# Optimization experiments

Hardware: AMD Instinct MI355X
Metric: run time of the kernel (lower is better)

The kernel has to match this reference:

```python
import jax, jax.numpy as jnp
import numpy as np

NEG_SLOPE = 0.2  # PyG GATConv default leaky_relu slope


def add_self_loops(src, dst, ea, n_nodes):
    # PyG add_self_loops with fill_value='mean': self-loop attr = mean of
    # incoming edge attrs per destination node (0 if no incoming edges).
    cnt = jax.ops.segment_sum(jnp.ones(dst.shape, ea.dtype), dst, num_segments=n_nodes)
    mean_ea = jax.ops.segment_sum(ea, dst, num_segments=n_nodes) / jnp.maximum(cnt, 1.0)[:, None]
    loop = jnp.arange(n_nodes, dtype=src.dtype)
    return (jnp.concatenate([src, loop]),
            jnp.concatenate([dst, loop]),
            jnp.concatenate([ea, mean_ea], axis=0))


def gat_conv(x, src, dst, ea, W, att_src, att_dst, We, att_edge, bias, heads, ch, concat):
    n = x.shape[0]
    xs = (x @ W).reshape(n, heads, ch)                      # [N,H,C]
    a_src = (xs * att_src).sum(-1)                          # [N,H]
    a_dst = (xs * att_dst).sum(-1)                          # [N,H]
    ea_p = (ea @ We).reshape(-1, heads, ch)                 # [E,H,C]
    a_e = (ea_p * att_edge).sum(-1)                         # [E,H]
    logits = jax.nn.leaky_relu(a_src[src] + a_dst[dst] + a_e, NEG_SLOPE)
    m = jax.ops.segment_max(logits, dst, num_segments=n)    # segment softmax over dst
    e = jnp.exp(logits - m[dst])
    denom = jax.ops.segment_sum(e, dst, num_segments=n)
    alpha = e / (denom[dst] + 1e-16)                        # [E,H]
    out = jax.ops.segment_sum(alpha[:, :, None] * xs[src], dst, num_segments=n)  # [N,H,C]
    out = out.reshape(n, heads * ch) if concat else out.mean(axis=1)
    return out + bias


def setup_inputs() -> dict:
    key = jax.random.key(0)
    ks = jax.random.split(key, 14)
    N, E, F_IN, H, C1, C2 = 50000, 800000, 128, 2, 64, 64
    s = 0.05
    return {
        "x": jax.random.normal(ks[0], (N, F_IN), jnp.float32),
        "edge_index": jax.random.randint(ks[1], (2, E), 0, N, jnp.int32),
        "edge_weight": jax.random.uniform(ks[2], (E,), jnp.float32),
        # layer 1 (heads=2, concat=True)
        "W1": jax.random.normal(ks[3], (F_IN, H * C1), jnp.float32) * s,
        "att_src1": jax.random.normal(ks[4], (1, H, C1), jnp.float32) * s,
        "att_dst1": jax.random.normal(ks[5], (1, H, C1), jnp.float32) * s,
        "We1": jax.random.normal(ks[6], (1, H * C1), jnp.float32) * s,
        "att_edge1": jax.random.normal(ks[7], (1, H, C1), jnp.float32) * s,
        "b1": jnp.zeros((H * C1,), jnp.float32),
        # layer 2 (heads=1, concat=False)
        "W2": jax.random.normal(ks[8], (H * C1, C2), jnp.float32) * s,
        "att_src2": jax.random.normal(ks[9], (1, 1, C2), jnp.float32) * s,
        "att_dst2": jax.random.normal(ks[10], (1, 1, C2), jnp.float32) * s,
        "We2": jax.random.normal(ks[11], (1, C2), jnp.float32) * s,
        "att_edge2": jax.random.normal(ks[12], (1, 1, C2), jnp.float32) * s,
        "b2": jnp.zeros((C2,), jnp.float32),
    }


def reference(x, edge_index, edge_weight, W1, att_src1, att_dst1, We1, att_edge1, b1,
              W2, att_src2, att_dst2, We2, att_edge2, b2):
    n = x.shape[0]
    ea = edge_weight[:, None]  # edge_dim=1
    src, dst, ea = add_self_loops(edge_index[0], edge_index[1], ea, n)
    h = gat_conv(x, src, dst, ea, W1, att_src1, att_dst1, We1, att_edge1, b1,
                 heads=2, ch=64, concat=True)
    h = jax.nn.elu(h)
    out = gat_conv(h, src, dst, ea, W2, att_src2, att_dst2, We2, att_edge2, b2,
                   heads=1, ch=64, concat=False)
    return out
```

## Files before the change

kernel.cpp:

```cpp
#include <hip/hip_runtime.h>
#include <math.h>

#define NEG_SLOPE 0.2f

typedef unsigned int u32;
typedef unsigned short u16;
typedef unsigned long long u64;

typedef __attribute__((ext_vector_type(8))) short short8;
typedef __attribute__((ext_vector_type(4))) float f32x4;

__device__ __forceinline__ float bf2f(u16 h) {
  union { u32 u; float f; } c; c.u = ((u32)h) << 16; return c.f;
}
__device__ __forceinline__ u16 f2bf(float f) {
  union { float f; u32 u; } c; c.f = f;
  return (u16)((c.u + 0x7FFFu + ((c.u >> 16) & 1u)) >> 16);
}

__global__ __launch_bounds__(256) void k_hist(const int* __restrict__ dst, int E, int epb,
                                              u32* __restrict__ hist) {
  __shared__ u32 h[256];
  h[threadIdx.x] = 0;
  __syncthreads();
  int b = blockIdx.x;
  int beg = b * epb, end = beg + epb; if (end > E) end = E;
  for (int i = beg + threadIdx.x; i < end; i += 256)
    atomicAdd(&h[(u32)dst[i] >> 8], 1u);
  __syncthreads();
  hist[threadIdx.x * 256 + b] = h[threadIdx.x];
}

__global__ __launch_bounds__(256) void k_scanrow(u32* __restrict__ hist, u32* __restrict__ btot) {
  int bkt = blockIdx.x, t = threadIdx.x;
  u32 orig = hist[bkt * 256 + t];
  u32 v = orig;
  #pragma unroll
  for (int off = 1; off < 64; off <<= 1) {
    u32 u_ = __shfl_up(v, off);
    if ((t & 63) >= off) v += u_;
  }
  __shared__ u32 ws[4];
  if ((t & 63) == 63) ws[t >> 6] = v;
  __syncthreads();
  u32 add = 0; int w = t >> 6;
  if (w > 0) add += ws[0];
  if (w > 1) add += ws[1];
  if (w > 2) add += ws[2];
  u32 incl = v + add;
  hist[bkt * 256 + t] = incl - orig;
  if (t == 255) btot[bkt] = incl;
}

__global__ __launch_bounds__(256) void k_scanb(const u32* __restrict__ btot, u32* __restrict__ bstart) {
  int t = threadIdx.x;
  u32 orig = btot[t];
  u32 v = orig;
  #pragma unroll
  for (int off = 1; off < 64; off <<= 1) {
    u32 u_ = __shfl_up(v, off);
    if ((t & 63) >= off) v += u_;
  }
  __shared__ u32 ws[4];
  if ((t & 63) == 63) ws[t >> 6] = v;
  __syncthreads();
  u32 add = 0; int w = t >> 6;
  if (w > 0) add += ws[0];
  if (w > 1) add += ws[1];
  if (w > 2) add += ws[2];
  u32 incl = v + add;
  bstart[t] = incl - orig;
  if (t == 255) bstart[256] = incl;
}

__global__ __launch_bounds__(256) void k_binscatter(const int* __restrict__ src,
                                                    const int* __restrict__ dst,
                                                    const float* __restrict__ ew,
                                                    const u32* __restrict__ hist,
                                                    const u32* __restrict__ bstart,
                                                    u64* __restrict__ stage, int E, int epb) {
  __shared__ u32 cur[256];
  int b = blockIdx.x;
  cur[threadIdx.x] = bstart[threadIdx.x] + hist[threadIdx.x * 256 + b];
  __syncthreads();
  int beg = b * epb, end = beg + epb; if (end > E) end = E;
  for (int i = beg + threadIdx.x; i < end; i += 256) {
    int d = dst[i];
    u32 bkt = (u32)d >> 8;
    u32 pos = atomicAdd(&cur[bkt], 1u);
    float w = ew[i];
    u32 wq = (u32)(w * 65536.0f); if (wq > 65535u) wq = 65535u;
    stage[pos] = ((u64)((u32)d & 255u) << 32) | ((u64)wq << 16) | (u64)(u32)src[i];
  }
}

__global__ __launch_bounds__(256) void k_bucket(const u64* __restrict__ stage,
                                                const u32* __restrict__ bstart,
                                                u32* __restrict__ col,
                                                u32* __restrict__ ninfo, int n) {
  int bkt = blockIdx.x;
  int beg = (int)bstart[bkt], end = (int)bstart[bkt + 1];
  __shared__ u32 cnt[256];
  __shared__ u32 wsum[256];
  __shared__ u32 cur[256];
  cnt[threadIdx.x] = 0; wsum[threadIdx.x] = 0; cur[threadIdx.x] = 0;
  __syncthreads();
  for (int i = beg + threadIdx.x; i < end; i += 256) {
    u64 sv = stage[i];
    u32 ln = (u32)(sv >> 32) & 255u;
    atomicAdd(&cnt[ln], 1u);
    atomicAdd(&wsum[ln], (u32)((sv >> 16) & 0xFFFFu));
  }
  __syncthreads();
  int v = (bkt << 8) + threadIdx.x;
  if (v < n) {
    u32 deg = cnt[threadIdx.x];
    float mean = ((float)wsum[threadIdx.x] * (1.0f / 65536.0f)) / (float)(deg > 1 ? deg : 1);
    u32 mq = (u32)(mean * 65536.0f); if (mq > 65535u) mq = 65535u;
    u32 dc = deg > 64u ? 64u : deg;
    ninfo[v] = (dc << 16) | mq;
  }
  __syncthreads();
  for (int i = beg + threadIdx.x; i < end; i += 256) {
    u64 sv = stage[i];
    u32 ln = (u32)(sv >> 32) & 255u;
    u32 rank = atomicAdd(&cur[ln], 1u);
    if (rank < 64u)
      col[((((u32)bkt << 8) + ln) << 6) + rank] = (u32)sv;
  }
}

template<int H>
__global__ void k_bfrag(const float* __restrict__ W, uint4* __restrict__ bfrag) {
  int tid = blockIdx.x * 256 + threadIdx.x;
  int f = tid >> 6, lane = tid & 63;
  const int NF = H * 4 * 4 * 2;
  if (f >= NF) return;
  int p = f & 1, t = (f >> 1) & 3, cg = f >> 3;
  int colc = 16 * cg + (lane & 15);
  int k0 = 32 * t + 8 * (lane >> 4);
  u16 v[8];
  #pragma unroll
  for (int j = 0; j < 8; j++) {
    float w = W[(size_t)(k0 + j) * (H * 64) + colc];
    u32 bits = __float_as_uint(w);
    if (p == 0) v[j] = (u16)(bits >> 16);
    else        v[j] = f2bf(w - __uint_as_float(bits & 0xffff0000u));
  }
  uint4 o = { (u32)v[0] | ((u32)v[1] << 16), (u32)v[2] | ((u32)v[3] << 16),
              (u32)v[4] | ((u32)v[5] << 16), (u32)v[6] | ((u32)v[7] << 16) };
  bfrag[f * 64 + lane] = o;
}

template<int H>
__global__ __launch_bounds__(256) void k_gemm_mfma(const float* __restrict__ A,
                                                   const uint4* __restrict__ bfrag,
                                                   u16* __restrict__ xs_bf,
                                                   const float* __restrict__ att_src,
                                                   const float* __restrict__ att_dst,
                                                   float* __restrict__ a_src_out,
                                                   float* __restrict__ a_dst_out,
                                                   int nrows) {
  const int NCG = H * 4;
  int lane = threadIdx.x & 63;
  int wv = threadIdx.x >> 6;
  int lrow = lane & 15, lk = lane >> 4;
  int r0 = blockIdx.x * 64 + wv * 16;
  int arow = r0 + lrow; if (arow > nrows - 1) arow = nrows - 1;
  const float* ap = A + (size_t)arow * 128;

  f32x4 acc[NCG];
  #pragma unroll
  for (int cg = 0; cg < NCG; cg++) acc[cg] = (f32x4){0.f, 0.f, 0.f, 0.f};

  #pragma unroll
  for (int t = 0; t < 4; t++) {
    float4 av0 = *(const float4*)(ap + 32 * t + 8 * lk);
    float4 av1 = *(const float4*)(ap + 32 * t + 8 * lk + 4);
    float af[8] = {av0.x, av0.y, av0.z, av0.w, av1.x, av1.y, av1.z, av1.w};
    short8 ahi, alo;
    #pragma unroll
    for (int j = 0; j < 8; j++) {
      u32 bits = __float_as_uint(af[j]);
      ahi[j] = (short)(bits >> 16);
      alo[j] = (short)f2bf(af[j] - __uint_as_float(bits & 0xffff0000u));
    }
    #pragma unroll
    for (int cg = 0; cg < NCG; cg++) {
      union { uint4 u; short8 s; } bh, bl;
      bh.u = bfrag[((cg * 4 + t) * 2 + 0) * 64 + lane];
      bl.u = bfrag[((cg * 4 + t) * 2 + 1) * 64 + lane];
      acc[cg] = __builtin_amdgcn_mfma_f32_16x16x32_bf16(ahi, bh.s, acc[cg], 0, 0, 0);
      acc[cg] = __builtin_amdgcn_mfma_f32_16x16x32_bf16(ahi, bl.s, acc[cg], 0, 0, 0);
      acc[cg] = __builtin_amdgcn_mfma_f32_16x16x32_bf16(alo, bh.s, acc[cg], 0, 0, 0);
    }
  }

  float ps[2][4], pd[2][4];
  #pragma unroll
  for (int h = 0; h < 2; h++)
    #pragma unroll
    for (int r = 0; r < 4; r++) { ps[h][r] = 0.f; pd[h][r] = 0.f; }

  #pragma unroll
  for (int cg = 0; cg < NCG; cg++) {
    int colbase = 16 * cg + lrow;
    float asv = att_src[colbase];
    float adv = att_dst[colbase];
    const int h = (H == 2) ? (cg >> 2) : 0;
    #pragma unroll
    for (int r = 0; r < 4; r++) {
      ps[h][r] += acc[cg][r] * asv;
      pd[h][r] += acc[cg][r] * adv;
      int row = r0 + 4 * lk + r;
      if (row < nrows) xs_bf[(size_t)row * (H * 64) + colbase] = f2bf(acc[cg][r]);
    }
  }
  #pragma unroll
  for (int h = 0; h < H; h++)
    #pragma unroll
    for (int r = 0; r < 4; r++)
      #pragma unroll
      for (int off = 8; off; off >>= 1) {
        ps[h][r] += __shfl_xor(ps[h][r], off);
        pd[h][r] += __shfl_xor(pd[h][r], off);
      }
  if (lrow == 0) {
    #pragma unroll
    for (int r = 0; r < 4; r++) {
      int row = r0 + 4 * lk + r;
      if (row < nrows) {
        #pragma unroll
        for (int h = 0; h < H; h++) {
          a_src_out[row * H + h] = ps[h][r];
          a_dst_out[row * H + h] = pd[h][r];
        }
      }
    }
  }
}

__global__ void k_scalars(const float* __restrict__ We1, const float* __restrict__ ae1,
                          const float* __restrict__ We2, const float* __restrict__ ae2,
                          float* __restrict__ out) {
  int t = threadIdx.x;
  if (t == 0) { float s = 0; for (int c = 0; c < 64; c++) s += We1[c] * ae1[c]; out[0] = s; }
  if (t == 1) { float s = 0; for (int c = 0; c < 64; c++) s += We1[64 + c] * ae1[64 + c]; out[1] = s; }
  if (t == 2) { float s = 0; for (int c = 0; c < 64; c++) s += We2[c] * ae2[c]; out[2] = s; }
}

__global__ __launch_bounds__(256) void k_agg1(const u32* __restrict__ ninfo,
                                              const u32* __restrict__ col,
                                              const float2* __restrict__ a_src,
                                              const float2* __restrict__ a_dst,
                                              const float* __restrict__ scal,
                                              const u16* __restrict__ xs_bf,
                                              const float* __restrict__ b1,
                                              float* __restrict__ h_out, int n) {
  int wid = (blockIdx.x * 256 + threadIdx.x) >> 4;
  int gl = threadIdx.x & 15;
  if (wid >= n) return;
  u32 nf = ninfo[wid];
  int deg = (int)(nf >> 16);
  float mean = (float)(nf & 0xFFFFu) * (1.0f / 65536.0f);
  float2 ad = a_dst[wid];
  float2 asv_s = a_src[wid];
  float sc0 = scal[0], sc1 = scal[1];
  bool hi = gl >= 8;
  float l0s = asv_s.x + ad.x + mean * sc0;
  float l1s = asv_s.y + ad.y + mean * sc1;
  l0s = l0s > 0.f ? l0s : NEG_SLOPE * l0s;
  l1s = l1s > 0.f ? l1s : NEG_SLOPE * l1s;
  float m0 = l0s, m1 = l1s, den0 = 1.f, den1 = 1.f;
  float acc[8];
  {
    uint4 q = *(const uint4*)&xs_bf[(size_t)wid * 128 + 8 * gl];
    acc[0] = bf2f((u16)q.x); acc[1] = bf2f((u16)(q.x >> 16));
    acc[2] = bf2f((u16)q.y); acc[3] = bf2f((u16)(q.y >> 16));
    acc[4] = bf2f((u16)q.z); acc[5] = bf2f((u16)(q.z >> 16));
    acc[6] = bf2f((u16)q.w); acc[7] = bf2f((u16)(q.w >> 16));
  }
  const u32* cw = col + ((u32)wid << 6);
  for (int p0 = 0; p0 < deg; p0 += 16) {
    int p = p0 + gl;
    bool act = p < deg;
    u32 sw = cw[act ? p : 0];
    int s = (int)(sw & 0xFFFFu);
    float w = (float)(sw >> 16) * (1.0f / 65536.0f);
    float2 asv = a_src[s];
    float l0 = asv.x + ad.x + w * sc0;
    float l1 = asv.y + ad.y + w * sc1;
    l0 = l0 > 0.f ? l0 : NEG_SLOPE * l0;
    l1 = l1 > 0.f ? l1 : NEG_SLOPE * l1;
    if (!act) { l0 = -1e30f; l1 = -1e30f; }
    float cm0 = l0, cm1 = l1;
    #pragma unroll
    for (int off = 8; off; off >>= 1) {
      cm0 = fmaxf(cm0, __shfl_xor(cm0, off, 16));
      cm1 = fmaxf(cm1, __shfl_xor(cm1, off, 16));
    }
    float nm0 = fmaxf(m0, cm0), nm1 = fmaxf(m1, cm1);
    float e0 = __expf(l0 - nm0), e1 = __expf(l1 - nm1);
    float cs0 = e0, cs1 = e1;
    #pragma unroll
    for (int off = 8; off; off >>= 1) {
      cs0 += __shfl_xor(cs0, off, 16);
      cs1 += __shfl_xor(cs1, off, 16);
    }
    float r0 = __expf(m0 - nm0), r1 = __expf(m1 - nm1);
    den0 = den0 * r0 + cs0;
    den1 = den1 * r1 + cs1;
    float rs = hi ? r1 : r0;
    #pragma unroll
    for (int f = 0; f < 8; f++) acc[f] *= rs;
    m0 = nm0; m1 = nm1;
    int cnt = deg - p0; if (cnt > 16) cnt = 16;
    for (int j = 0; j < cnt; j++) {
      float a0 = __shfl(e0, j, 16);
      float a1 = __shfl(e1, j, 16);
      int   sj = __shfl(s, j, 16);
      uint4 q = *(const uint4*)&xs_bf[(size_t)sj * 128 + 8 * gl];
      float al = hi ? a1 : a0;
      acc[0] += al * bf2f((u16)q.x); acc[1] += al * bf2f((u16)(q.x >> 16));
      acc[2] += al * bf2f((u16)q.y); acc[3] += al * bf2f((u16)(q.y >> 16));
      acc[4] += al * bf2f((u16)q.z); acc[5] += al * bf2f((u16)(q.z >> 16));
      acc[6] += al * bf2f((u16)q.w); acc[7] += al * bf2f((u16)(q.w >> 16));
    }
  }
  float inv = 1.f / ((hi ? den1 : den0) + 1e-16f);
  float4 blo = *(const float4*)&b1[8 * gl];
  float4 bhi = *(const float4*)&b1[8 * gl + 4];
  float o[8];
  o[0] = acc[0] * inv + blo.x; o[1] = acc[1] * inv + blo.y;
  o[2] = acc[2] * inv + blo.z; o[3] = acc[3] * inv + blo.w;
  o[4] = acc[4] * inv + bhi.x; o[5] = acc[5] * inv + bhi.y;
  o[6] = acc[6] * inv + bhi.z; o[7] = acc[7] * inv + bhi.w;
  #pragma unroll
  for (int f = 0; f < 8; f++) o[f] = o[f] > 0.f ? o[f] : expm1f(o[f]);
  float* dst = &h_out[(size_t)wid * 128 + 8 * gl];
  *(float4*)dst = make_float4(o[0], o[1], o[2], o[3]);
  *(float4*)(dst + 4) = make_float4(o[4], o[5], o[6], o[7]);
}

__global__ __launch_bounds__(256) void k_agg2(const u32* __restrict__ ninfo,
                                              const u32* __restrict__ col,
                                              const float* __restrict__ a_src,
                                              const float* __restrict__ a_dst,
                                              const float* __restrict__ scal,
                                              const u16* __restrict__ xs_bf,
                                              const float* __restrict__ b2,
                                              float* __restrict__ out, int n) {
  int wid = (blockIdx.x * 256 + threadIdx.x) >> 3;
  int gl = threadIdx.x & 7;
  if (wid >= n) return;
  u32 nf = ninfo[wid];
  int deg = (int)(nf >> 16);
  float mean = (float)(nf & 0xFFFFu) * (1.0f / 65536.0f);
  float adv = a_dst[wid];
  float sc = scal[2];
  float ls = a_src[wid] + adv + mean * sc;
  ls = ls > 0.f ? ls : NEG_SLOPE * ls;
  float m = ls, den = 1.f;
  float acc[8];
  {
    uint4 q = *(const uint4*)&xs_bf[(size_t)wid * 64 + 8 * gl];
    acc[0] = bf2f((u16)q.x); acc[1] = bf2f((u16)(q.x >> 16));
    acc[2] = bf2f((u16)q.y); acc[3] = bf2f((u16)(q.y >> 16));
    acc[4] = bf2f((u16)q.z); acc[5] = bf2f((u16)(q.z >> 16));
    acc[6] = bf2f((u16)q.w); acc[7] = bf2f((u16)(q.w >> 16));
  }
  const u32* cw = col + ((u32)wid << 6);
  for (int p0 = 0; p0 < deg; p0 += 8) {
    int p = p0 + gl;
    bool act = p < deg;
    u32 sw = cw[act ? p : 0];
    int s = (int)(sw & 0xFFFFu);
    float w = (float)(sw >> 16) * (1.0f / 65536.0f);
    float l = a_src[s] + adv + w * sc;
    l = l > 0.f ? l : NEG_SLOPE * l;
    if (!act) l = -1e30f;
    float cm = l;
    #pragma unroll
    for (int off = 4; off; off >>= 1) cm = fmaxf(cm, __shfl_xor(cm, off, 8));
    float nm = fmaxf(m, cm);
    float e = __expf(l - nm);
    float cs = e;
    #pragma unroll
    for (int off = 4; off; off >>= 1) cs += __shfl_xor(cs, off, 8);
    float r = __expf(m - nm);
    den = den * r + cs;
    #pragma unroll
    for (int f = 0; f < 8; f++) acc[f] *= r;
    m = nm;
    int cnt = deg - p0; if (cnt > 8) cnt = 8;
    for (int j = 0; j < cnt; j++) {
      float aj = __shfl(e, j, 8);
      int   sj = __shfl(s, j, 8);
      uint4 q = *(const uint4*)&xs_bf[(size_t)sj * 64 + 8 * gl];
      acc[0] += aj * bf2f((u16)q.x); acc[1] += aj * bf2f((u16)(q.x >> 16));
      acc[2] += aj * bf2f((u16)q.y); acc[3] += aj * bf2f((u16)(q.y >> 16));
      acc[4] += aj * bf2f((u16)q.z); acc[5] += aj * bf2f((u16)(q.z >> 16));
      acc[6] += aj * bf2f((u16)q.w); acc[7] += aj * bf2f((u16)(q.w >> 16));
    }
  }
  float inv = 1.f / (den + 1e-16f);
  float4 blo = *(const float4*)&b2[8 * gl];
  float4 bhi = *(const float4*)&b2[8 * gl + 4];
  float* dst = &out[(size_t)wid * 64 + 8 * gl];
  *(float4*)dst = make_float4(acc[0] * inv + blo.x, acc[1] * inv + blo.y,
                              acc[2] * inv + blo.z, acc[3] * inv + blo.w);
  *(float4*)(dst + 4) = make_float4(acc[4] * inv + bhi.x, acc[5] * inv + bhi.y,
                                    acc[6] * inv + bhi.z, acc[7] * inv + bhi.w);
}

extern "C" void kernel_launch(void* const* d_in, const int* in_sizes, int n_in,
                              void* d_out, int out_size, void* d_ws, size_t ws_size,
                              hipStream_t stream) {
  const float* x   = (const float*)d_in[0];
  const int*   ei  = (const int*)d_in[1];
  const float* ew  = (const float*)d_in[2];
  const float* W1  = (const float*)d_in[3];
  const float* as1 = (const float*)d_in[4];
  const float* ad1 = (const float*)d_in[5];
  const float* We1 = (const float*)d_in[6];
  const float* ae1 = (const float*)d_in[7];
  const float* b1  = (const float*)d_in[8];
  const float* W2  = (const float*)d_in[9];
  const float* as2 = (const float*)d_in[10];
  const float* ad2 = (const float*)d_in[11];
  const float* We2 = (const float*)d_in[12];
  const float* ae2 = (const float*)d_in[13];
  const float* b2  = (const float*)d_in[14];

  const int n = in_sizes[0] / 128;
  const int E = in_sizes[1] / 2;
  const int epb = (E + 255) / 256;
  const int nbk = (n + 255) >> 8;

  char* wsb = (char*)d_ws;
  size_t off = 0;
  auto alloc = [&](size_t bytes) -> void* {
    void* p = wsb + off; off += (bytes + 255) & ~(size_t)255; return p;
  };
  u32*   hist    = (u32*)  alloc((size_t)256 * 256 * 4);
  u32*   btot    = (u32*)  alloc((size_t)256 * 4);
  u32*   bstart  = (u32*)  alloc((size_t)257 * 4);
  u64*   stage   = (u64*)  alloc((size_t)E * 8);
  u32*   col     = (u32*)  alloc((size_t)n * 64 * 4);
  u32*   ninfo   = (u32*)  alloc((size_t)n * 4);
  uint4* bfrag1  = (uint4*)alloc((size_t)64 * 64 * 16);
  uint4* bfrag2  = (uint4*)alloc((size_t)32 * 64 * 16);
  u16*   xs_bf   = (u16*)  alloc((size_t)n * 128 * 2);
  float* h1      = (float*)alloc((size_t)n * 128 * 4);
  float* a_src1v = (float*)alloc((size_t)n * 2 * 4);
  float* a_dst1v = (float*)alloc((size_t)n * 2 * 4);
  float* a_src2v = (float*)alloc((size_t)n * 4);
  float* a_dst2v = (float*)alloc((size_t)n * 4);
  float* scal    = (float*)alloc(64);
  if (off > ws_size) return;

  dim3 B(256);
  k_hist<<<dim3(256), B, 0, stream>>>(ei + E, E, epb, hist);
  k_scanrow<<<dim3(256), B, 0, stream>>>(hist, btot);
  k_scanb<<<dim3(1), B, 0, stream>>>(btot, bstart);
  k_binscatter<<<dim3(256), B, 0, stream>>>(ei, ei + E, ew, hist, bstart, stage, E, epb);
  k_bucket<<<dim3(nbk), B, 0, stream>>>(stage, bstart, col, ninfo, n);
  k_bfrag<2><<<dim3(16), B, 0, stream>>>(W1, bfrag1);
  k_bfrag<1><<<dim3(8), B, 0, stream>>>(W2, bfrag2);
  k_scalars<<<1, 64, 0, stream>>>(We1, ae1, We2, ae2, scal);
  k_gemm_mfma<2><<<dim3((n + 63) / 64), B, 0, stream>>>(x, bfrag1, xs_bf, as1, ad1,
                                                        a_src1v, a_dst1v, n);
  k_agg1<<<dim3((n + 15) / 16), B, 0, stream>>>(ninfo, col,
                                                (const float2*)a_src1v,
                                                (const float2*)a_dst1v,
                                                scal, xs_bf, b1, h1, n);
  k_gemm_mfma<1><<<dim3((n + 63) / 64), B, 0, stream>>>(h1, bfrag2, xs_bf, as2, ad2,
                                                        a_src2v, a_dst2v, n);
  k_agg2<<<dim3((n + 31) / 32), B, 0, stream>>>(ninfo, col, a_src2v, a_dst2v,
                                                scal, xs_bf, b2, (float*)d_out, n);
}
```

Measured before the change: 141.1 us.

## Fuse bucket count and scatter passes; unroll gather loops by two

The bucketing kernel now packs the degree count and the quantized weight sum into a single shared atomic per node. The returned old value gives the rank directly, which removes the second pass over the staged edges and one barrier. Both GAT aggregation kernels unroll the neighbor gather by two so that two independent row loads are in flight at once, raising memory-level parallelism. The packed counter limits the weight sum to 24 bits and the rank to 8 bits, so a node with about 256 or more incoming edges would overflow.

```diff
diff --git a/kernel.cpp b/kernel.cpp
--- a/kernel.cpp
+++ b/kernel.cpp
@@ -100,33 +100,27 @@
                                                 u32* __restrict__ ninfo, int n) {
   int bkt = blockIdx.x;
   int beg = (int)bstart[bkt], end = (int)bstart[bkt + 1];
-  __shared__ u32 cnt[256];
-  __shared__ u32 wsum[256];
-  __shared__ u32 cur[256];
-  cnt[threadIdx.x] = 0; wsum[threadIdx.x] = 0; cur[threadIdx.x] = 0;
+  __shared__ u32 pk[256];
+  pk[threadIdx.x] = 0;
   __syncthreads();
   for (int i = beg + threadIdx.x; i < end; i += 256) {
     u64 sv = stage[i];
     u32 ln = (u32)(sv >> 32) & 255u;
-    atomicAdd(&cnt[ln], 1u);
-    atomicAdd(&wsum[ln], (u32)((sv >> 16) & 0xFFFFu));
+    u32 wq = (u32)((sv >> 16) & 0xFFFFu);
+    u32 old = atomicAdd(&pk[ln], (1u << 24) | wq);
+    u32 rank = old >> 24;
+    if (rank < 64u)
+      col[((((u32)bkt << 8) + ln) << 6) + rank] = (u32)sv;
   }
   __syncthreads();
   int v = (bkt << 8) + threadIdx.x;
   if (v < n) {
-    u32 deg = cnt[threadIdx.x];
-    float mean = ((float)wsum[threadIdx.x] * (1.0f / 65536.0f)) / (float)(deg > 1 ? deg : 1);
+    u32 p = pk[threadIdx.x];
+    u32 deg = p >> 24;
+    float mean = ((float)(p & 0xFFFFFFu) * (1.0f / 65536.0f)) / (float)(deg > 1 ? deg : 1);
     u32 mq = (u32)(mean * 65536.0f); if (mq > 65535u) mq = 65535u;
     u32 dc = deg > 64u ? 64u : deg;
     ninfo[v] = (dc << 16) | mq;
-  }
-  __syncthreads();
-  for (int i = beg + threadIdx.x; i < end; i += 256) {
-    u64 sv = stage[i];
-    u32 ln = (u32)(sv >> 32) & 255u;
-    u32 rank = atomicAdd(&cur[ln], 1u);
-    if (rank < 64u)
-      col[((((u32)bkt << 8) + ln) << 6) + rank] = (u32)sv;
   }
 }
 
@@ -315,11 +309,29 @@
     for (int f = 0; f < 8; f++) acc[f] *= rs;
     m0 = nm0; m1 = nm1;
     int cnt = deg - p0; if (cnt > 16) cnt = 16;
-    for (int j = 0; j < cnt; j++) {
-      float a0 = __shfl(e0, j, 16);
-      float a1 = __shfl(e1, j, 16);
-      int   sj = __shfl(s, j, 16);
+    int j = 0;
+    for (; j + 2 <= cnt; j += 2) {
+      int sj0 = __shfl(s, j, 16);
+      int sj1 = __shfl(s, j + 1, 16);
+      uint4 qa = *(const uint4*)&xs_bf[(size_t)sj0 * 128 + 8 * gl];
+      uint4 qb = *(const uint4*)&xs_bf[(size_t)sj1 * 128 + 8 * gl];
+      float a0 = __shfl(e0, j, 16), a1 = __shfl(e1, j, 16);
+      float b0 = __shfl(e0, j + 1, 16), b1 = __shfl(e1, j + 1, 16);
+      float ala = hi ? a1 : a0;
+      float alb = hi ? b1 : b0;
+      acc[0] += ala * bf2f((u16)qa.x); acc[1] += ala * bf2f((u16)(qa.x >> 16));
+      acc[2] += ala * bf2f((u16)qa.y); acc[3] += ala * bf2f((u16)(qa.y >> 16));
+      acc[4] += ala * bf2f((u16)qa.z); acc[5] += ala * bf2f((u16)(qa.z >> 16));
+      acc[6] += ala * bf2f((u16)qa.w); acc[7] += ala * bf2f((u16)(qa.w >> 16));
+      acc[0] += alb * bf2f((u16)qb.x); acc[1] += alb * bf2f((u16)(qb.x >> 16));
+      acc[2] += alb * bf2f((u16)qb.y); acc[3] += alb * bf2f((u16)(qb.y >> 16));
+      acc[4] += alb * bf2f((u16)qb.z); acc[5] += alb * bf2f((u16)(qb.z >> 16));
+      acc[6] += alb * bf2f((u16)qb.w); acc[7] += alb * bf2f((u16)(qb.w >> 16));
+    }
+    if (j < cnt) {
+      int sj = __shfl(s, j, 16);
       uint4 q = *(const uint4*)&xs_bf[(size_t)sj * 128 + 8 * gl];
+      float a0 = __shfl(e0, j, 16), a1 = __shfl(e1, j, 16);
       float al = hi ? a1 : a0;
       acc[0] += al * bf2f((u16)q.x); acc[1] += al * bf2f((u16)(q.x >> 16));
       acc[2] += al * bf2f((u16)q.y); acc[3] += al * bf2f((u16)(q.y >> 16));
@@ -393,10 +405,27 @@
     for (int f = 0; f < 8; f++) acc[f] *= r;
     m = nm;
     int cnt = deg - p0; if (cnt > 8) cnt = 8;
-    for (int j = 0; j < cnt; j++) {
+    int j = 0;
+    for (; j + 2 <= cnt; j += 2) {
+      int sj0 = __shfl(s, j, 8);
+      int sj1 = __shfl(s, j + 1, 8);
+      uint4 qa = *(const uint4*)&xs_bf[(size_t)sj0 * 64 + 8 * gl];
+      uint4 qb = *(const uint4*)&xs_bf[(size_t)sj1 * 64 + 8 * gl];
+      float aja = __shfl(e, j, 8);
+      float ajb = __shfl(e, j + 1, 8);
+      acc[0] += aja * bf2f((u16)qa.x); acc[1] += aja * bf2f((u16)(qa.x >> 16));
+      acc[2] += aja * bf2f((u16)qa.y); acc[3] += aja * bf2f((u16)(qa.y >> 16));
+      acc[4] += aja * bf2f((u16)qa.z); acc[5] += aja * bf2f((u16)(qa.z >> 16));
+      acc[6] += aja * bf2f((u16)qa.w); acc[7] += aja * bf2f((u16)(qa.w >> 16));
+      acc[0] += ajb * bf2f((u16)qb.x); acc[1] += ajb * bf2f((u16)(qb.x >> 16));
+      acc[2] += ajb * bf2f((u16)qb.y); acc[3] += ajb * bf2f((u16)(qb.y >> 16));
+      acc[4] += ajb * bf2f((u16)qb.z); acc[5] += ajb * bf2f((u16)(qb.z >> 16));
+      acc[6] += ajb * bf2f((u16)qb.w); acc[7] += ajb * bf2f((u16)(qb.w >> 16));
+    }
+    if (j < cnt) {
+      int sj = __shfl(s, j, 8);
+      uint4 q = *(const uint4*)&xs_bf[(size_t)sj * 64 + 8 * gl];
       float aj = __shfl(e, j, 8);
-      int   sj = __shfl(s, j, 8);
-      uint4 q = *(const uint4*)&xs_bf[(size_t)sj * 64 + 8 * gl];
       acc[0] += aj * bf2f((u16)q.x); acc[1] += aj * bf2f((u16)(q.x >> 16));
       acc[2] += aj * bf2f((u16)q.y); acc[3] += aj * bf2f((u16)(q.y >> 16));
       acc[4] += aj * bf2f((u16)q.z); acc[5] += aj * bf2f((u16)(q.z >> 16));
```

After: 136.0 us. 3.6% less time.
